# Kernel optimization log

Hardware: AMD Instinct MI355X
Metric: run time of the kernel (lower is better)

## Reference

```python
import jax, jax.numpy as jnp
import numpy as np

B, S, D_IN = 4, 2048, 512
H, D_OUT = 8, 64


def setup_inputs() -> dict:
    key = jax.random.key(0)
    k1, k2, k3 = jax.random.split(key, 3)
    x = jax.random.normal(k1, (B, S, D_IN), dtype=jnp.float32)
    # matches torch init: w ~ U(-0.8, 0.8), wo ~ U(-1, 1)
    w = jax.random.uniform(k2, (H, 3, D_IN, D_OUT), dtype=jnp.float32, minval=-0.8, maxval=0.8)
    wo = jax.random.uniform(k3, (H * D_OUT, D_OUT), dtype=jnp.float32, minval=-1.0, maxval=1.0)
    return {"x": x, "w": w, "wo": wo}


def reference(x, w, wo):
    d_out = w.shape[-1]
    # batched per-head projections: [B, H, S, D_OUT]
    q = jnp.einsum('bsi,hio->bhso', x, w[:, 0])
    k = jnp.einsum('bsi,hio->bhso', x, w[:, 1])
    v = jnp.einsum('bsi,hio->bhso', x, w[:, 2])
    scores = jnp.einsum('bhso,bhto->bhst', q, k) / jnp.sqrt(jnp.asarray(d_out, x.dtype))
    attn = jax.nn.softmax(scores, axis=-1)
    o = jnp.einsum('bhst,bhto->bhso', attn, v)  # [B, H, S, D_OUT]
    # concat heads along feature dim (head order matches torch cat order)
    o = jnp.transpose(o, (0, 2, 1, 3)).reshape(x.shape[0], x.shape[1], -1)
    return jnp.matmul(o, wo)
```

## Files before the change

### kernel.cpp

```cpp
#include <hip/hip_runtime.h>
#include <cstdint>
#include <cstddef>

#define S_LEN 2048
#define DIN   512
#define DOUT  64
#define NB    4
#define NH    8

typedef __attribute__((ext_vector_type(8))) short bf16x8;
typedef __attribute__((ext_vector_type(8))) _Float16 f16x8;
typedef __attribute__((ext_vector_type(4))) float f32x4;
typedef __attribute__((ext_vector_type(16))) float f32x16;

static __device__ __forceinline__ f32x4 mfma16(bf16x8 a, bf16x8 b, f32x4 c) {
    return __builtin_amdgcn_mfma_f32_16x16x32_bf16(a, b, c, 0, 0, 0);
}
static __device__ __forceinline__ f32x16 mfma32h(f16x8 a, f16x8 b, f32x16 c) {
    return __builtin_amdgcn_mfma_f32_32x32x16_f16(a, b, c, 0, 0, 0);
}

static __device__ __forceinline__ uint16_t f2bf(float x) {
    uint32_t u = __builtin_bit_cast(uint32_t, x);
    u += 0x7fffu + ((u >> 16) & 1u);
    return (uint16_t)(u >> 16);
}
static __device__ __forceinline__ float bf2f(uint16_t h) {
    uint32_t u = ((uint32_t)h) << 16;
    return __builtin_bit_cast(float, u);
}
static __device__ __forceinline__ uint32_t cvt_pk_bf16(float lo, float hi) {
    uint32_t r;
    asm("v_cvt_pk_bf16_f32 %0, %1, %2" : "=v"(r) : "v"(lo), "v"(hi));
    return r;
}
static __device__ __forceinline__ uint32_t cvt_pkrtz_f16(float lo, float hi) {
    return __builtin_bit_cast(uint32_t, __builtin_amdgcn_cvt_pkrtz(lo, hi));
}

typedef const __attribute__((address_space(1))) void* as1p;
typedef __attribute__((address_space(3))) void* as3p;
static __device__ __forceinline__ void gload_lds16(const void* g, void* l) {
    __builtin_amdgcn_global_load_lds((as1p)g, (as3p)l, 16, 0, 0);
}

__global__ __launch_bounds__(256) void prep_w(
    const float* __restrict__ w, const float* __restrict__ wo,
    uint16_t* __restrict__ whiT, uint16_t* __restrict__ wloT,
    uint16_t* __restrict__ woT)
{
    __shared__ float tile[64][65];
    const int blk = blockIdx.x;
    const int t = threadIdx.x;
    const int tq = t >> 6, tr = t & 63;

    if (blk < 192) {
        const int hp = blk >> 3, i0 = (blk & 7) * 64;
        const int p = hp % 3;
        const float s = (p == 0) ? 0.18033688011112042f : 1.0f;
        const float* __restrict__ src = w + (size_t)hp * (DIN * DOUT);
        #pragma unroll
        for (int r = 0; r < 16; ++r) {
            const int ir = r * 4 + tq;
            tile[ir][tr] = src[(size_t)(i0 + ir) * DOUT + tr];
        }
        __syncthreads();
        uint16_t* __restrict__ dh = whiT + (size_t)hp * (DOUT * DIN);
        uint16_t* __restrict__ dl = wloT + (size_t)hp * (DOUT * DIN);
        #pragma unroll
        for (int r = 0; r < 16; ++r) {
            const int o = r * 4 + tq;
            const float v = tile[tr][o] * s;
            const uint16_t hi = f2bf(v);
            dh[(size_t)o * DIN + i0 + tr] = hi;
            dl[(size_t)o * DIN + i0 + tr] = f2bf(v - bf2f(hi));
        }
    } else {
        const int i0 = (blk - 192) * 64;
        #pragma unroll
        for (int r = 0; r < 16; ++r) {
            const int ir = r * 4 + tq;
            tile[ir][tr] = wo[(size_t)(i0 + ir) * DOUT + tr];
        }
        __syncthreads();
        #pragma unroll
        for (int r = 0; r < 16; ++r) {
            const int o = r * 4 + tq;
            woT[(size_t)o * DIN + i0 + tr] = f2bf(tile[tr][o]);
        }
    }
}

__global__ __launch_bounds__(256) void split_x(
    const float* __restrict__ x, uint16_t* __restrict__ xhi, uint16_t* __restrict__ xlo)
{
    const size_t idx = ((size_t)blockIdx.x * 256 + threadIdx.x) * 8;
    const float4 a = *(const float4*)(x + idx);
    const float4 b = *(const float4*)(x + idx + 4);
    const float xv[8] = {a.x, a.y, a.z, a.w, b.x, b.y, b.z, b.w};
    union { uint16_t u[8]; uint4 v; } H, L;
    #pragma unroll
    for (int j = 0; j < 8; ++j) {
        const uint16_t hi = f2bf(xv[j]);
        H.u[j] = hi;
        L.u[j] = f2bf(xv[j] - bf2f(hi));
    }
    *(uint4*)(xhi + idx) = H.v;
    *(uint4*)(xlo + idx) = L.v;
}

__global__ __launch_bounds__(256) void gemm_qkv(
    const uint16_t* __restrict__ xhi, const uint16_t* __restrict__ xlo,
    const uint16_t* __restrict__ whiT, const uint16_t* __restrict__ wloT,
    uint16_t* __restrict__ qf, uint16_t* __restrict__ kf,
    uint16_t* __restrict__ vT)
{
    __shared__ __align__(16) uint16_t lds[2 * 128 * 64];

    const int bid = blockIdx.x;
    const int xcd = bid & 7, wi = bid >> 3;
    const int mt = xcd * 8 + wi / 12, nt = wi % 12;
    const int m0 = mt * 128, n0 = nt * 128;
    const int tid = threadIdx.x;
    const int l = tid & 63, w = tid >> 6;
    const int g = l >> 4, lm = l & 15;
    const int wm = w >> 1, wn = w & 1;

    const f32x4 Z = {0.f, 0.f, 0.f, 0.f};
    f32x4 acc[4][4];
    #pragma unroll
    for (int a = 0; a < 4; ++a)
        #pragma unroll
        for (int b = 0; b < 4; ++b) acc[a][b] = Z;

    int srow[4], scol[4];
    #pragma unroll
    for (int i = 0; i < 4; ++i) {
        const int c = i * 256 + tid;
        srow[i] = c >> 3;
        scol[i] = ((c & 7) * 8) ^ ((srow[i] & 7) << 3);
    }

    for (int kt = 0; kt < 24; ++kt) {
        const int k0 = (kt & 7) * 64;
        const uint16_t* __restrict__ As = (kt < 16) ? xhi : xlo;
        const uint16_t* __restrict__ Bs = (kt >= 8 && kt < 16) ? wloT : whiT;
        #pragma unroll
        for (int i = 0; i < 4; ++i) {
            const int c8 = (i * 256 + tid) * 8;
            gload_lds16(As + (size_t)(m0 + srow[i]) * DIN + k0 + scol[i], &lds[c8]);
            gload_lds16(Bs + (size_t)(n0 + srow[i]) * DIN + k0 + scol[i], &lds[128 * 64 + c8]);
        }
        asm volatile("s_waitcnt vmcnt(0)" ::: "memory");
        __syncthreads();

        bf16x8 af[4][2];
        #pragma unroll
        for (int mi = 0; mi < 4; ++mi) {
            const int r = wm * 64 + mi * 16 + lm;
            const int rb = r * 128;
            #pragma unroll
            for (int kk = 0; kk < 2; ++kk) {
                const int cb = (kk * 64 + g * 16) ^ ((r & 7) << 4);
                af[mi][kk] = *(const bf16x8*)((const char*)lds + rb + cb);
            }
        }
        #pragma unroll
        for (int ni = 0; ni < 4; ++ni) {
            const int r = wn * 64 + ni * 16 + lm;
            const int rb = 128 * 64 * 2 + r * 128;
            bf16x8 bfr[2];
            #pragma unroll
            for (int kk = 0; kk < 2; ++kk) {
                const int cb = (kk * 64 + g * 16) ^ ((r & 7) << 4);
                bfr[kk] = *(const bf16x8*)((const char*)lds + rb + cb);
            }
            #pragma unroll
            for (int mi = 0; mi < 4; ++mi) {
                acc[mi][ni] = mfma16(af[mi][0], bfr[0], acc[mi][ni]);
                acc[mi][ni] = mfma16(af[mi][1], bfr[1], acc[mi][ni]);
            }
        }
        __syncthreads();
    }

    #pragma unroll
    for (int ni = 0; ni < 4; ++ni) {
        const int n = n0 + wn * 64 + ni * 16 + lm;
        const int hp = n >> 6, o = n & 63;
        const int h = hp / 3, p = hp - h * 3;
        if (p < 2) {
            uint16_t* __restrict__ dst = (p == 0) ? qf : kf;
            #pragma unroll
            for (int mi = 0; mi < 4; ++mi) {
                #pragma unroll
                for (int j = 0; j < 4; ++j) {
                    const int m = m0 + wm * 64 + mi * 16 + 4 * g + j;
                    const int b = m >> 11, s = m & 2047;
                    const size_t idx = ((size_t)(b * NH + h) * S_LEN + s) * DOUT + o;
                    const _Float16 hv = (_Float16)acc[mi][ni][j];
                    dst[idx] = __builtin_bit_cast(uint16_t, hv);
                }
            }
        } else {
            #pragma unroll
            for (int mi = 0; mi < 4; ++mi) {
                const int m = m0 + wm * 64 + mi * 16 + 4 * g;
                const int b = m >> 11, s = m & 2047;
                union { _Float16 h[4]; uint2 u; } pk;
                pk.h[0] = (_Float16)acc[mi][ni][0];
                pk.h[1] = (_Float16)acc[mi][ni][1];
                pk.h[2] = (_Float16)acc[mi][ni][2];
                pk.h[3] = (_Float16)acc[mi][ni][3];
                *(uint2*)(vT + ((size_t)((b * NH + h) * DOUT + o)) * S_LEN + s) = pk.u;
            }
        }
    }
}

__global__ __launch_bounds__(256, 2) void attn_fwd(
    const uint16_t* __restrict__ qf, const uint16_t* __restrict__ kf,
    const uint16_t* __restrict__ vT, uint16_t* __restrict__ oc)
{
    __shared__ __align__(16) char smem[32768];
    char* __restrict__ vbufs = smem + 16384;

    const int bid = blockIdx.x;
    const int qt = (bid >> 3) & 15, bh = (bid & 7) + 8 * (bid >> 7);
    const int tid = threadIdx.x;
    const int l = tid & 63, wq = tid >> 6;
    const int L = l >> 5, lq = l & 31;
    const size_t base = (size_t)bh * (S_LEN * DOUT);

    const int c0 = tid, c1 = tid + 256;
    const int kr0 = c0 & 31,        do0 = ((c0 >> 5) & 7) << 3;
    const int kr1 = 32 + (c1 & 31), do1 = ((c1 >> 5) & 7) << 3;

    const int qrow = qt * 128 + wq * 32 + lq;
    const uint16_t* qp = qf + base + (size_t)qrow * DOUT;
    f16x8 qv[4];
    #pragma unroll
    for (int dsub = 0; dsub < 4; ++dsub)
        qv[dsub] = *(const f16x8*)(qp + dsub * 16 + L * 8);

    f32x16 Zv;
    #pragma unroll
    for (int r = 0; r < 16; ++r) Zv[r] = 0.f;
    f32x16 Oa[2] = {Zv, Zv};
    float m_run = -INFINITY, l_run = 0.f;

    auto qk_step = [&](const char* kb2, f32x16* dst) {
        #pragma unroll
        for (int ks = 0; ks < 2; ++ks) {
            f32x16 s = Zv;
            #pragma unroll
            for (int dsub = 0; dsub < 4; ++dsub) {
                const uint32_t off = (uint32_t)(((ks * 4 + dsub) << 10) + (l << 4));
                const f16x8 kfr = *(const f16x8*)(kb2 + off);
                s = mfma32h(kfr, qv[dsub], s);
            }
            dst[ks] = s;
        }
    };

    gload_lds16(kf + base + (size_t)kr0 * DOUT + do0, smem + c0 * 16);
    gload_lds16(kf + base + (size_t)kr1 * DOUT + do1, smem + c1 * 16);
    gload_lds16(kf + base + (size_t)(64 + kr0) * DOUT + do0, smem + 8192 + c0 * 16);
    gload_lds16(kf + base + (size_t)(64 + kr1) * DOUT + do1, smem + 8192 + c1 * 16);
    gload_lds16(vT + base + (size_t)kr0 * S_LEN + do0, vbufs + c0 * 16);
    gload_lds16(vT + base + (size_t)kr1 * S_LEN + do1, vbufs + c1 * 16);
    asm volatile("s_waitcnt vmcnt(0)" ::: "memory");
    __builtin_amdgcn_s_barrier();
    __builtin_amdgcn_sched_barrier(0);

    f32x16 saA[2], saB[2];
    qk_step(smem, saA);

    auto iter = [&](int kt, f32x16* sa, f32x16* sb) {
        asm volatile("s_waitcnt vmcnt(0)" ::: "memory");
        __builtin_amdgcn_s_barrier();
        __builtin_amdgcn_sched_barrier(0);

        {
            char* __restrict__ kn = smem + (kt & 1) * 8192;
            const int sK = (kt < 30) ? (kt + 2) * 64 : 0;
            gload_lds16(kf + base + (size_t)(sK + kr0) * DOUT + do0, kn + c0 * 16);
            gload_lds16(kf + base + (size_t)(sK + kr1) * DOUT + do1, kn + c1 * 16);
            char* __restrict__ vn = vbufs + ((kt + 1) & 1) * 8192;
            const int sV = (kt < 31) ? (kt + 1) * 64 : 0;
            gload_lds16(vT + base + (size_t)kr0 * S_LEN + sV + do0, vn + c0 * 16);
            gload_lds16(vT + base + (size_t)kr1 * S_LEN + sV + do1, vn + c1 * 16);
        }

        qk_step(smem + ((kt + 1) & 1) * 8192, sb);

        float mx[16];
        #pragma unroll
        for (int r = 0; r < 16; ++r) mx[r] = fmaxf(sa[0][r], sa[1][r]);
        #pragma unroll
        for (int st = 8; st >= 1; st >>= 1)
            #pragma unroll
            for (int r = 0; r < st; ++r) mx[r] = fmaxf(mx[r], mx[r + st]);
        float pmax = mx[0];
        pmax = fmaxf(pmax, __shfl_xor(pmax, 32));

        if (!__all(pmax - m_run <= 8.f)) {
            const float m_new = fmaxf(m_run, pmax);
            const float alpha = __builtin_amdgcn_exp2f(m_run - m_new);
            m_run = m_new;
            #pragma unroll
            for (int r = 0; r < 16; ++r) { Oa[0][r] *= alpha; Oa[1][r] *= alpha; }
            l_run *= alpha;
        }

        #pragma unroll
        for (int ks = 0; ks < 2; ++ks)
            #pragma unroll
            for (int r = 0; r < 16; ++r)
                sa[ks][r] = __builtin_amdgcn_exp2f(sa[ks][r] - m_run);

        float sm[16];
        #pragma unroll
        for (int r = 0; r < 16; ++r) sm[r] = sa[0][r] + sa[1][r];
        #pragma unroll
        for (int st = 8; st >= 1; st >>= 1)
            #pragma unroll
            for (int r = 0; r < st; ++r) sm[r] += sm[r + st];
        float lsum = sm[0];
        lsum += __shfl_xor(lsum, 32);
        l_run += lsum;

        f16x8 pfrag[4];
        #pragma unroll
        for (int ks = 0; ks < 2; ++ks) {
            uint32_t a0 = cvt_pkrtz_f16(sa[ks][0], sa[ks][1]);
            uint32_t a1 = cvt_pkrtz_f16(sa[ks][2], sa[ks][3]);
            uint32_t a2 = cvt_pkrtz_f16(sa[ks][4], sa[ks][5]);
            uint32_t a3 = cvt_pkrtz_f16(sa[ks][6], sa[ks][7]);
            asm volatile("v_permlane32_swap_b32 %0, %1" : "+v"(a0), "+v"(a2));
            asm volatile("v_permlane32_swap_b32 %0, %1" : "+v"(a1), "+v"(a3));
            union { uint32_t w[4]; f16x8 v; } u;
            u.w[0] = a0; u.w[1] = a1; u.w[2] = a2; u.w[3] = a3;
            pfrag[2 * ks] = u.v;
            uint32_t b0 = cvt_pkrtz_f16(sa[ks][8],  sa[ks][9]);
            uint32_t b1 = cvt_pkrtz_f16(sa[ks][10], sa[ks][11]);
            uint32_t b2 = cvt_pkrtz_f16(sa[ks][12], sa[ks][13]);
            uint32_t b3 = cvt_pkrtz_f16(sa[ks][14], sa[ks][15]);
            asm volatile("v_permlane32_swap_b32 %0, %1" : "+v"(b0), "+v"(b2));
            asm volatile("v_permlane32_swap_b32 %0, %1" : "+v"(b1), "+v"(b3));
            union { uint32_t w[4]; f16x8 v; } u2;
            u2.w[0] = b0; u2.w[1] = b1; u2.w[2] = b2; u2.w[3] = b3;
            pfrag[2 * ks + 1] = u2.v;
        }

        const char* __restrict__ vb = vbufs + (kt & 1) * 8192;
        __builtin_amdgcn_s_setprio(1);
        #pragma unroll
        for (int dh = 0; dh < 2; ++dh) {
            #pragma unroll
            for (int kc = 0; kc < 4; ++kc) {
                const uint32_t off = (uint32_t)(((dh * 4 + kc) << 10) + (l << 4));
                const f16x8 vv = *(const f16x8*)(vb + off);
                Oa[dh] = mfma32h(vv, pfrag[kc], Oa[dh]);
            }
        }
        __builtin_amdgcn_s_setprio(0);
    };

    for (int kt2 = 0; kt2 < 16; ++kt2) {
        iter(2 * kt2,     saA, saB);
        iter(2 * kt2 + 1, saB, saA);
    }
    asm volatile("s_waitcnt vmcnt(0)" ::: "memory");

    const int b = bh >> 3, hh = bh & 7;
    const float li = 1.f / l_run;
    const int srow = qt * 128 + wq * 32 + lq;
    const size_t rbase = ((size_t)b * S_LEN + srow) * (NH * DOUT) + hh * DOUT;
    #pragma unroll
    for (int dh = 0; dh < 2; ++dh) {
        #pragma unroll
        for (int rq = 0; rq < 4; ++rq) {
            const int d0 = dh * 32 + rq * 8 + L * 4;
            uint2 val;
            val.x = cvt_pk_bf16(Oa[dh][rq * 4 + 0] * li, Oa[dh][rq * 4 + 1] * li);
            val.y = cvt_pk_bf16(Oa[dh][rq * 4 + 2] * li, Oa[dh][rq * 4 + 3] * li);
            *(uint2*)(oc + rbase + d0) = val;
        }
    }
}

__global__ __launch_bounds__(256) void oproj(
    const uint16_t* __restrict__ oc, const uint16_t* __restrict__ woT,
    float* __restrict__ out)
{
    const int mt = blockIdx.x;
    const int tid = threadIdx.x;
    const int l = tid & 63, w = tid >> 6;
    const int g = l >> 4, lm = l & 15;
    const int m0 = mt * 64 + w * 16;
    const f32x4 Z = {0.f, 0.f, 0.f, 0.f};
    f32x4 acc[4] = {Z, Z, Z, Z};
    const uint16_t* __restrict__ arow = oc + (size_t)(m0 + lm) * (NH * DOUT);
    for (int kc = 0; kc < 16; ++kc) {
        const bf16x8 a = *(const bf16x8*)(arow + kc * 32 + g * 8);
        #pragma unroll
        for (int nt = 0; nt < 4; ++nt) {
            const bf16x8 bfr = *(const bf16x8*)(woT + (size_t)(nt * 16 + lm) * (NH * DOUT) + kc * 32 + g * 8);
            acc[nt] = mfma16(a, bfr, acc[nt]);
        }
    }
    #pragma unroll
    for (int nt = 0; nt < 4; ++nt)
        #pragma unroll
        for (int j = 0; j < 4; ++j)
            out[(size_t)(m0 + 4 * g + j) * DOUT + nt * 16 + lm] = acc[nt][j];
}

extern "C" void kernel_launch(void* const* d_in, const int* in_sizes, int n_in,
                              void* d_out, int out_size, void* d_ws, size_t ws_size,
                              hipStream_t stream) {
    const float* x  = (const float*)d_in[0];
    const float* w  = (const float*)d_in[1];
    const float* wo = (const float*)d_in[2];
    float* out = (float*)d_out;

    char* ws = (char*)d_ws;
    uint16_t* qf   = (uint16_t*)(ws);
    uint16_t* kf   = (uint16_t*)(ws + 8388608);
    uint16_t* vT   = (uint16_t*)(ws + 16777216);
    uint16_t* xhi  = (uint16_t*)(ws + 25165824);
    uint16_t* xlo  = (uint16_t*)(ws + 33554432);
    uint16_t* whiT = (uint16_t*)(ws + 41943040);
    uint16_t* wloT = (uint16_t*)(ws + 43515904);
    uint16_t* woT  = (uint16_t*)(ws + 45088768);
    uint16_t* oc   = xhi;

    hipLaunchKernelGGL(prep_w, dim3(200), dim3(256), 0, stream, w, wo, whiT, wloT, woT);
    hipLaunchKernelGGL(split_x, dim3(2048), dim3(256), 0, stream, x, xhi, xlo);
    hipLaunchKernelGGL(gemm_qkv, dim3(768), dim3(256), 0, stream,
                       xhi, xlo, whiT, wloT, qf, kf, vT);
    hipLaunchKernelGGL(attn_fwd, dim3(512), dim3(256), 0, stream,
                       qf, kf, vT, oc);
    hipLaunchKernelGGL(oproj, dim3(128), dim3(256), 0, stream, oc, woT, out);
}
```

Before: 131.9 us.

## Fuse three split-bf16 GEMM passes into one K loop with shared tiles

The QKV GEMM previously ran 24 K-iterations that reloaded x-hi or x-lo and w-hi or w-lo tiles separately for the hi*hi, hi*lo and lo*hi products. It now runs 8 iterations, loading all four tiles into a 64KB LDS buffer at once and issuing six MFMAs per tile pair. This reuses the x-hi and w-hi tiles across products and cuts barrier and loop overhead. The cost is double the LDS footprint and more live fragment registers, which may limit occupancy even with the added launch-bounds hint of 2 blocks.

```diff
diff --git a/kernel.cpp b/kernel.cpp
--- a/kernel.cpp
+++ b/kernel.cpp
@@ -109,13 +109,13 @@
     *(uint4*)(xlo + idx) = L.v;
 }
 
-__global__ __launch_bounds__(256) void gemm_qkv(
+__global__ __launch_bounds__(256, 2) void gemm_qkv(
     const uint16_t* __restrict__ xhi, const uint16_t* __restrict__ xlo,
     const uint16_t* __restrict__ whiT, const uint16_t* __restrict__ wloT,
     uint16_t* __restrict__ qf, uint16_t* __restrict__ kf,
     uint16_t* __restrict__ vT)
 {
-    __shared__ __align__(16) uint16_t lds[2 * 128 * 64];
+    __shared__ __align__(16) uint16_t lds[4 * 128 * 64];
 
     const int bid = blockIdx.x;
     const int xcd = bid & 7, wi = bid >> 3;
@@ -141,20 +141,22 @@
         scol[i] = ((c & 7) * 8) ^ ((srow[i] & 7) << 3);
     }
 
-    for (int kt = 0; kt < 24; ++kt) {
-        const int k0 = (kt & 7) * 64;
-        const uint16_t* __restrict__ As = (kt < 16) ? xhi : xlo;
-        const uint16_t* __restrict__ Bs = (kt >= 8 && kt < 16) ? wloT : whiT;
+    for (int kt = 0; kt < 8; ++kt) {
+        const int k0 = kt * 64;
         #pragma unroll
         for (int i = 0; i < 4; ++i) {
             const int c8 = (i * 256 + tid) * 8;
-            gload_lds16(As + (size_t)(m0 + srow[i]) * DIN + k0 + scol[i], &lds[c8]);
-            gload_lds16(Bs + (size_t)(n0 + srow[i]) * DIN + k0 + scol[i], &lds[128 * 64 + c8]);
+            const size_t aoff = (size_t)(m0 + srow[i]) * DIN + k0 + scol[i];
+            const size_t boff = (size_t)(n0 + srow[i]) * DIN + k0 + scol[i];
+            gload_lds16(xhi  + aoff, &lds[c8]);
+            gload_lds16(xlo  + aoff, &lds[128 * 64 + c8]);
+            gload_lds16(whiT + boff, &lds[2 * 128 * 64 + c8]);
+            gload_lds16(wloT + boff, &lds[3 * 128 * 64 + c8]);
         }
         asm volatile("s_waitcnt vmcnt(0)" ::: "memory");
         __syncthreads();
 
-        bf16x8 af[4][2];
+        bf16x8 ah[4][2], al[4][2];
         #pragma unroll
         for (int mi = 0; mi < 4; ++mi) {
             const int r = wm * 64 + mi * 16 + lm;
@@ -162,23 +164,29 @@
             #pragma unroll
             for (int kk = 0; kk < 2; ++kk) {
                 const int cb = (kk * 64 + g * 16) ^ ((r & 7) << 4);
-                af[mi][kk] = *(const bf16x8*)((const char*)lds + rb + cb);
+                ah[mi][kk] = *(const bf16x8*)((const char*)lds + rb + cb);
+                al[mi][kk] = *(const bf16x8*)((const char*)lds + 16384 + rb + cb);
             }
         }
         #pragma unroll
         for (int ni = 0; ni < 4; ++ni) {
             const int r = wn * 64 + ni * 16 + lm;
-            const int rb = 128 * 64 * 2 + r * 128;
-            bf16x8 bfr[2];
+            const int rb = r * 128;
+            bf16x8 bh[2], bl[2];
             #pragma unroll
             for (int kk = 0; kk < 2; ++kk) {
                 const int cb = (kk * 64 + g * 16) ^ ((r & 7) << 4);
-                bfr[kk] = *(const bf16x8*)((const char*)lds + rb + cb);
+                bh[kk] = *(const bf16x8*)((const char*)lds + 32768 + rb + cb);
+                bl[kk] = *(const bf16x8*)((const char*)lds + 49152 + rb + cb);
             }
             #pragma unroll
             for (int mi = 0; mi < 4; ++mi) {
-                acc[mi][ni] = mfma16(af[mi][0], bfr[0], acc[mi][ni]);
-                acc[mi][ni] = mfma16(af[mi][1], bfr[1], acc[mi][ni]);
+                acc[mi][ni] = mfma16(ah[mi][0], bh[0], acc[mi][ni]);
+                acc[mi][ni] = mfma16(ah[mi][1], bh[1], acc[mi][ni]);
+                acc[mi][ni] = mfma16(ah[mi][0], bl[0], acc[mi][ni]);
+                acc[mi][ni] = mfma16(ah[mi][1], bl[1], acc[mi][ni]);
+                acc[mi][ni] = mfma16(al[mi][0], bh[0], acc[mi][ni]);
+                acc[mi][ni] = mfma16(al[mi][1], bh[1], acc[mi][ni]);
             }
         }
         __syncthreads();
```

After: 114.3 us. 13.3% less time.
